# Kernel optimization log

Measured on AMD Instinct MI355X. Metric: run time of the kernel, lower is better.

The kernel has to match this reference:

```python
import jax, jax.numpy as jnp
import numpy as np

DIM = 1024
N_HEADS = 16
HEAD_DIM = DIM // N_HEADS
EPS = 1e-05
ROPE_BASE = 1000000.0


def apply_rope(x, base=ROPE_BASE):
    # x: [b, seq, heads, head_dim]
    b, seq, n_heads, dim = x.shape
    half = dim // 2
    i = jnp.arange(half)
    theta = 1.0 / base ** (2 * i / dim)
    pos = jnp.arange(seq)
    angles = pos[:, None] * theta[None, :]            # [seq, half]
    cos = jnp.cos(angles)[None, :, None, :]           # [1, seq, 1, half]
    sin = jnp.sin(angles)[None, :, None, :]
    x1, x2 = jnp.split(x, 2, axis=-1)
    return jnp.concatenate([x1 * cos - x2 * sin, x1 * sin + x2 * cos], axis=-1)


def setup_inputs() -> dict:
    key = jax.random.key(0)
    ks = jax.random.split(key, 6)
    b, seq = 2, 2048
    scale = 1.0 / np.sqrt(DIM)
    x = jax.random.normal(ks[0], (b, seq, DIM), dtype=jnp.float32)
    w_norm = jnp.ones((DIM,), dtype=jnp.float32)
    Wq = jax.random.normal(ks[1], (DIM, DIM), dtype=jnp.float32) * scale
    Wk = jax.random.normal(ks[2], (DIM, DIM), dtype=jnp.float32) * scale
    Wv = jax.random.normal(ks[3], (DIM, DIM), dtype=jnp.float32) * scale
    Wo = jax.random.normal(ks[4], (DIM, DIM), dtype=jnp.float32) * scale
    return {"x": x, "w_norm": w_norm, "Wq": Wq, "Wk": Wk, "Wv": Wv, "Wo": Wo}


def reference(x, w_norm, Wq, Wk, Wv, Wo):
    b, seq, d = x.shape
    # RMSNorm
    rms = jnp.sqrt(jnp.mean(x * x, axis=-1, keepdims=True) + EPS)
    x_norm = x / rms * w_norm
    # QKV projections (Dense without bias: y = x @ W)
    q = (x_norm @ Wq).reshape(b, seq, N_HEADS, HEAD_DIM)
    k = (x_norm @ Wk).reshape(b, seq, N_HEADS, HEAD_DIM)
    v = (x_norm @ Wv).reshape(b, seq, N_HEADS, HEAD_DIM)
    q = apply_rope(q)
    k = apply_rope(k)
    # Causal attention with full [b,h,t,s] scores (faithful to source)
    scores = jnp.einsum('bthd,bshd->bhts', q, k) / jnp.sqrt(jnp.float32(HEAD_DIM))
    causal = jnp.triu(jnp.full((seq, seq), -jnp.inf, dtype=scores.dtype), k=1)
    scores = scores + causal[None, None, :, :]
    attn = jax.nn.softmax(scores, axis=-1)
    out = jnp.einsum('bhts,bshd->bthd', attn, v).reshape(b, seq, d)
    return out @ Wo
```

## Files before the change

### kernel.cpp

```cpp
#include <hip/hip_runtime.h>

#define DIM 1024
#define SEQ 2048
#define BATCH 2
#define NHEADS 16
#define HD 64
#define ROWS (BATCH * SEQ)

typedef __bf16 bf16x8 __attribute__((ext_vector_type(8)));
typedef __bf16 bf16x4 __attribute__((ext_vector_type(4)));
typedef float f32x4 __attribute__((ext_vector_type(4)));
typedef float f32x16 __attribute__((ext_vector_type(16)));
typedef unsigned u32x4 __attribute__((ext_vector_type(4)));

__device__ __forceinline__ f32x4 f4zero() {
    f32x4 z = {0.f, 0.f, 0.f, 0.f};
    return z;
}

__device__ __forceinline__ unsigned cvtpk(float lo, float hi) {
    unsigned r;
    asm("v_cvt_pk_bf16_f32 %0, %1, %2" : "=v"(r) : "v"(lo), "v"(hi));
    return r;
}

__device__ __forceinline__ void pl32swap(unsigned& a, unsigned& b) {
    asm volatile("v_permlane32_swap_b32 %0, %1" : "+v"(a), "+v"(b));
}

#define GLOAD_LDS16(g, l)                                                                  \
    __builtin_amdgcn_global_load_lds((const __attribute__((address_space(1))) void*)(g),   \
                                     (__attribute__((address_space(3))) void*)(l), 16, 0, 0)

__global__ __launch_bounds__(256) void rmsnorm_bf16(const float* __restrict__ x,
                                                    const float* __restrict__ w,
                                                    __bf16* __restrict__ xn) {
    int row = blockIdx.x;
    int t = threadIdx.x;
    float4 v = ((const float4*)(x + (size_t)row * DIM))[t];
    float ss = v.x * v.x + v.y * v.y + v.z * v.z + v.w * v.w;
#pragma unroll
    for (int off = 1; off < 64; off <<= 1) ss += __shfl_xor(ss, off);
    __shared__ float red[4];
    if ((t & 63) == 0) red[t >> 6] = ss;
    __syncthreads();
    ss = red[0] + red[1] + red[2] + red[3];
    float scale = rsqrtf(ss * (1.0f / DIM) + 1e-5f);
    float4 wv = ((const float4*)w)[t];
    bf16x4 o;
    o[0] = (__bf16)(v.x * scale * wv.x);
    o[1] = (__bf16)(v.y * scale * wv.y);
    o[2] = (__bf16)(v.z * scale * wv.z);
    o[3] = (__bf16)(v.w * scale * wv.w);
    *(bf16x4*)(xn + (size_t)row * DIM + t * 4) = o;
}

__global__ __launch_bounds__(256) void wcvt_kernel(const float* __restrict__ Wq,
                                                   const float* __restrict__ Wk,
                                                   const float* __restrict__ Wv,
                                                   const float* __restrict__ Wo,
                                                   __bf16* tq, __bf16* tk, __bf16* tv, __bf16* to_) {
    int z = blockIdx.z;
    const float* W = z == 0 ? Wq : z == 1 ? Wk : z == 2 ? Wv : Wo;
    __bf16* T = z == 0 ? tq : z == 1 ? tk : z == 2 ? tv : to_;
    __shared__ float tile[32][33];
    int n0 = blockIdx.x * 32, k0 = blockIdx.y * 32;
    int tx = threadIdx.x & 31, ty = threadIdx.x >> 5;
#pragma unroll
    for (int j = 0; j < 32; j += 8) tile[ty + j][tx] = W[(size_t)(k0 + ty + j) * DIM + n0 + tx];
    __syncthreads();
#pragma unroll
    for (int j = 0; j < 32; j += 8)
        T[(size_t)(n0 + ty + j) * DIM + k0 + tx] = (__bf16)tile[tx][ty + j];
}

__global__ __launch_bounds__(256) void rope_table_kernel(float* __restrict__ cosT,
                                                         float* __restrict__ sinT) {
    int idx = blockIdx.x * 256 + threadIdx.x;
    int s = idx >> 5, i = idx & 31;
    float e = (2.0f * (float)i) / 64.0f;
    float theta = 1.0f / powf(1000000.0f, e);
    float ang = (float)s * theta;
    cosT[idx] = cosf(ang);
    sinT[idx] = sinf(ang);
}

__device__ __forceinline__ void gemm_core(const __bf16* __restrict__ A,
                                          const __bf16* __restrict__ Bt,
                                          int K, __bf16* As, __bf16* Bs,
                                          f32x4 (&acc)[4][4], int row0, int col0) {
    int tid = threadIdx.x;
    int w = tid >> 6, l = tid & 63, l15 = l & 15, g = l >> 4;
    int wr = (w >> 1) << 6, wc = (w & 1) << 6;

    int sr0 = tid >> 2;
    int sr1 = 64 + (tid >> 2);
    int lc0 = (((tid & 3) ^ ((tid >> 3) & 3)) << 3);
    const __bf16* gA0 = A + (size_t)(row0 + sr0) * K + lc0;
    const __bf16* gA1 = A + (size_t)(row0 + sr1) * K + lc0;
    const __bf16* gB0 = Bt + (size_t)(col0 + sr0) * K + lc0;
    const __bf16* gB1 = Bt + (size_t)(col0 + sr1) * K + lc0;
    __bf16* lA0 = As + w * 512;
    __bf16* lA1 = As + 2048 + w * 512;
    __bf16* lB0 = Bs + w * 512;
    __bf16* lB1 = Bs + 2048 + w * 512;

    int rca = ((g ^ ((l15 >> 1) & 3)) << 3);

#pragma unroll
    for (int i = 0; i < 4; ++i)
#pragma unroll
        for (int j = 0; j < 4; ++j) acc[i][j] = f4zero();

    for (int k0 = 0; k0 < K; k0 += 32) {
        __syncthreads();
        GLOAD_LDS16(gA0 + k0, lA0);
        GLOAD_LDS16(gA1 + k0, lA1);
        GLOAD_LDS16(gB0 + k0, lB0);
        GLOAD_LDS16(gB1 + k0, lB1);
        __syncthreads();

        bf16x8 af[4], bfr[4];
#pragma unroll
        for (int i = 0; i < 4; ++i) af[i] = *(const bf16x8*)&As[(wr + i * 16 + l15) * 32 + rca];
#pragma unroll
        for (int j = 0; j < 4; ++j) bfr[j] = *(const bf16x8*)&Bs[(wc + j * 16 + l15) * 32 + rca];
        __builtin_amdgcn_s_setprio(1);
#pragma unroll
        for (int i = 0; i < 4; ++i)
#pragma unroll
            for (int j = 0; j < 4; ++j)
                acc[i][j] = __builtin_amdgcn_mfma_f32_16x16x32_bf16(af[i], bfr[j], acc[i][j], 0, 0, 0);
        __builtin_amdgcn_s_setprio(0);
    }
}

__global__ __launch_bounds__(256) void gemm_qkv_kernel(const __bf16* __restrict__ xn,
                                                       const __bf16* __restrict__ wq,
                                                       const __bf16* __restrict__ wk,
                                                       const __bf16* __restrict__ wv,
                                                       __bf16* __restrict__ qo,
                                                       __bf16* __restrict__ ko,
                                                       __bf16* __restrict__ vt,
                                                       const float* __restrict__ cosT,
                                                       const float* __restrict__ sinT) {
    __shared__ __bf16 As[128 * 32];
    __shared__ __bf16 Bs[128 * 32];
    int bid = blockIdx.x;
    int tid = threadIdx.x;
    int w = tid >> 6, l = tid & 63, l15 = l & 15, g = l >> 4;
    int wr = (w >> 1) << 6, wc = (w & 1) << 6;
    f32x4 acc[4][4];

    if (bid < 512) {
        int z = bid >> 8, t = bid & 255;
        int col0 = (t & 7) << 7, row0 = (t >> 3) << 7;
        gemm_core(xn, z ? wk : wq, DIM, As, Bs, acc, row0, col0);
        __bf16* C = z ? ko : qo;
        int colbase = col0 + wc;
#pragma unroll
        for (int i = 0; i < 4; ++i) {
#pragma unroll
            for (int r = 0; r < 4; ++r) {
                int row = row0 + wr + i * 16 + g * 4 + r;
                int s = row & (SEQ - 1);
#pragma unroll
                for (int j = 0; j < 2; ++j) {
                    float c = cosT[s * 32 + j * 16 + l15];
                    float sn = sinT[s * 32 + j * 16 + l15];
                    float x1 = acc[i][j][r], x2 = acc[i][j + 2][r];
                    C[(size_t)row * DIM + colbase + j * 16 + l15] = (__bf16)(x1 * c - x2 * sn);
                    C[(size_t)row * DIM + colbase + (j + 2) * 16 + l15] = (__bf16)(x1 * sn + x2 * c);
                }
            }
        }
    } else {
        int t = bid - 512;
        int b = t >> 7, r7 = t & 127;
        int row0 = (r7 >> 4) << 7;
        int col0 = (r7 & 15) << 7;
        gemm_core(wv, xn + (size_t)b * SEQ * DIM, DIM, As, Bs, acc, row0, col0);
        __bf16* C = vt + (size_t)b * (NHEADS * HD) * SEQ;
#pragma unroll
        for (int i = 0; i < 4; ++i)
#pragma unroll
            for (int j = 0; j < 4; ++j)
#pragma unroll
                for (int r = 0; r < 4; ++r) {
                    int row = row0 + wr + i * 16 + g * 4 + r;
                    int col = col0 + wc + j * 16 + l15;
                    C[(size_t)row * SEQ + col] = (__bf16)acc[i][j][r];
                }
    }
}

__global__ __launch_bounds__(256) void gemm_out_kernel(const __bf16* __restrict__ ctx,
                                                       const __bf16* __restrict__ wo,
                                                       float* __restrict__ out) {
    __shared__ __bf16 As[128 * 32];
    __shared__ __bf16 Bs[128 * 32];
    int row0 = (int)blockIdx.y << 7, col0 = (int)blockIdx.x << 7;
    f32x4 acc[4][4];
    gemm_core(ctx, wo, DIM, As, Bs, acc, row0, col0);
    int tid = threadIdx.x;
    int w = tid >> 6, l = tid & 63, l15 = l & 15, g = l >> 4;
    int wr = (w >> 1) << 6, wc = (w & 1) << 6;
#pragma unroll
    for (int i = 0; i < 4; ++i)
#pragma unroll
        for (int j = 0; j < 4; ++j)
#pragma unroll
            for (int r = 0; r < 4; ++r) {
                int row = row0 + wr + i * 16 + g * 4 + r;
                int col = col0 + wc + j * 16 + l15;
                out[(size_t)row * DIM + col] = acc[i][j][r];
            }
}

__global__ __launch_bounds__(128) void attn_mfma_kernel(const __bf16* __restrict__ q,
                                                        const __bf16* __restrict__ k,
                                                        const __bf16* __restrict__ vt,
                                                        __bf16* __restrict__ ctx) {
    int bh = blockIdx.x;
    int qb = 31 - (int)blockIdx.y;
    int b = bh >> 4, h = bh & 15;
    __shared__ __bf16 Ks[64][72];
    __shared__ __bf16 Vs[64][72];
    int tid = threadIdx.x, w = tid >> 6, l = tid & 63;
    int l31 = l & 31, hi = l >> 5;
    size_t hoff = (size_t)(b * SEQ) * DIM + h * HD;
    const __bf16* vth = vt + (size_t)bh * HD * SEQ;
    int qw0 = qb * 64 + w * 32;
    int qrow = qw0 + l31;
    int nst = qb + 1;

    bf16x8 qf[4];
    const float c2 = 0.125f * 1.44269504f;
#pragma unroll
    for (int g = 0; g < 4; ++g) {
        bf16x8 t0 = *(const bf16x8*)&q[hoff + (size_t)qrow * DIM + g * 16 + hi * 8];
#pragma unroll
        for (int e = 0; e < 8; ++e) qf[g][e] = (__bf16)((float)t0[e] * c2);
    }

    f32x16 oA, oB;
#pragma unroll
    for (int r = 0; r < 16; ++r) {
        oA[r] = 0.f;
        oB[r] = 0.f;
    }
    float m_run = -1e30f, l_run = 0.f;

    int sr = tid >> 3, sc = (tid & 7) * 8;
    bf16x8 rk[4], rv[4];
#pragma unroll
    for (int c = 0; c < 4; ++c) {
        rk[c] = *(const bf16x8*)&k[hoff + (size_t)(c * 16 + sr) * DIM + sc];
        rv[c] = *(const bf16x8*)&vth[(size_t)(c * 16 + sr) * SEQ + sc];
    }

    for (int st = 0; st < nst; ++st) {
        int s0 = st << 6;
        __syncthreads();
#pragma unroll
        for (int c = 0; c < 4; ++c) {
            *(bf16x8*)&Ks[c * 16 + sr][sc] = rk[c];
            *(bf16x8*)&Vs[c * 16 + sr][sc] = rv[c];
        }
        __syncthreads();
        if (st + 1 < nst) {
            int sn = s0 + 64;
#pragma unroll
            for (int c = 0; c < 4; ++c) {
                rk[c] = *(const bf16x8*)&k[hoff + (size_t)(sn + c * 16 + sr) * DIM + sc];
                rv[c] = *(const bf16x8*)&vth[(size_t)(c * 16 + sr) * SEQ + sn + sc];
            }
        }

        f32x16 sa, sb;
#pragma unroll
        for (int r = 0; r < 16; ++r) {
            sa[r] = 0.f;
            sb[r] = 0.f;
        }
        __builtin_amdgcn_s_setprio(1);
#pragma unroll
        for (int g = 0; g < 4; ++g) {
            bf16x8 ka = *(const bf16x8*)&Ks[l31][g * 16 + hi * 8];
            bf16x8 kb2 = *(const bf16x8*)&Ks[32 + l31][g * 16 + hi * 8];
            sa = __builtin_amdgcn_mfma_f32_32x32x16_bf16(ka, qf[g], sa, 0, 0, 0);
            sb = __builtin_amdgcn_mfma_f32_32x32x16_bf16(kb2, qf[g], sb, 0, 0, 0);
        }
        __builtin_amdgcn_s_setprio(0);

        if (s0 + 63 > qw0) {
#pragma unroll
            for (int r = 0; r < 16; ++r) {
                int kg = s0 + (r & 3) + 8 * (r >> 2) + 4 * hi;
                if (kg > qrow) sa[r] = -1e30f;
                if (kg + 32 > qrow) sb[r] = -1e30f;
            }
        }

        float lmax = -3e38f;
#pragma unroll
        for (int r = 0; r < 16; ++r) lmax = fmaxf(lmax, fmaxf(sa[r], sb[r]));
        if (!__all(lmax <= m_run + 10.0f)) {
            float omax = fmaxf(lmax, __shfl_xor(lmax, 32));
            float m_new = fmaxf(m_run, omax);
            float alpha = exp2f(m_run - m_new);
            l_run *= alpha;
#pragma unroll
            for (int r = 0; r < 16; ++r) {
                oA[r] *= alpha;
                oB[r] *= alpha;
            }
            m_run = m_new;
        }
        float ls = 0.f;
#pragma unroll
        for (int r = 0; r < 16; ++r) {
            sa[r] = exp2f(sa[r] - m_run);
            ls += sa[r];
            sb[r] = exp2f(sb[r] - m_run);
            ls += sb[r];
        }
        l_run += ls + __shfl_xor(ls, 32);

        bf16x8 pa[4];
#pragma unroll
        for (int g = 0; g < 2; ++g) {
            unsigned a_ = cvtpk(sa[8 * g + 0], sa[8 * g + 1]);
            unsigned b_ = cvtpk(sa[8 * g + 4], sa[8 * g + 5]);
            pl32swap(a_, b_);
            unsigned c_ = cvtpk(sa[8 * g + 2], sa[8 * g + 3]);
            unsigned d_ = cvtpk(sa[8 * g + 6], sa[8 * g + 7]);
            pl32swap(c_, d_);
            u32x4 t4 = {a_, c_, b_, d_};
            pa[g] = __builtin_bit_cast(bf16x8, t4);
        }
#pragma unroll
        for (int g = 0; g < 2; ++g) {
            unsigned a_ = cvtpk(sb[8 * g + 0], sb[8 * g + 1]);
            unsigned b_ = cvtpk(sb[8 * g + 4], sb[8 * g + 5]);
            pl32swap(a_, b_);
            unsigned c_ = cvtpk(sb[8 * g + 2], sb[8 * g + 3]);
            unsigned d_ = cvtpk(sb[8 * g + 6], sb[8 * g + 7]);
            pl32swap(c_, d_);
            u32x4 t4 = {a_, c_, b_, d_};
            pa[2 + g] = __builtin_bit_cast(bf16x8, t4);
        }

        __builtin_amdgcn_s_setprio(1);
#pragma unroll
        for (int ks = 0; ks < 4; ++ks) {
            bf16x8 va = *(const bf16x8*)&Vs[l31][ks * 16 + hi * 8];
            bf16x8 vb2 = *(const bf16x8*)&Vs[32 + l31][ks * 16 + hi * 8];
            oA = __builtin_amdgcn_mfma_f32_32x32x16_bf16(va, pa[ks], oA, 0, 0, 0);
            oB = __builtin_amdgcn_mfma_f32_32x32x16_bf16(vb2, pa[ks], oB, 0, 0, 0);
        }
        __builtin_amdgcn_s_setprio(0);
    }

    float inv = 1.0f / l_run;
#pragma unroll
    for (int rr = 0; rr < 16; rr += 4) {
        int d = 8 * (rr >> 2) + 4 * hi;
        uint2 pA = {cvtpk(oA[rr] * inv, oA[rr + 1] * inv), cvtpk(oA[rr + 2] * inv, oA[rr + 3] * inv)};
        uint2 pB = {cvtpk(oB[rr] * inv, oB[rr + 1] * inv), cvtpk(oB[rr + 2] * inv, oB[rr + 3] * inv)};
        *(uint2*)&ctx[hoff + (size_t)qrow * DIM + d] = pA;
        *(uint2*)&ctx[hoff + (size_t)qrow * DIM + 32 + d] = pB;
    }
}

extern "C" void kernel_launch(void* const* d_in, const int* in_sizes, int n_in,
                              void* d_out, int out_size, void* d_ws, size_t ws_size,
                              hipStream_t stream) {
    const float* x = (const float*)d_in[0];
    const float* w_norm = (const float*)d_in[1];
    const float* Wq = (const float*)d_in[2];
    const float* Wk = (const float*)d_in[3];
    const float* Wv = (const float*)d_in[4];
    const float* Wo = (const float*)d_in[5];
    float* out = (float*)d_out;
    char* w8 = (char*)d_ws;

    __bf16* xn = (__bf16*)(w8);
    __bf16* wtq = (__bf16*)(w8 + (8ull << 20));
    __bf16* wtk = (__bf16*)(w8 + (10ull << 20));
    __bf16* wtv = (__bf16*)(w8 + (12ull << 20));
    __bf16* wto = (__bf16*)(w8 + (14ull << 20));
    __bf16* qb = (__bf16*)(w8 + (16ull << 20));
    __bf16* kb = (__bf16*)(w8 + (24ull << 20));
    __bf16* vtb = (__bf16*)(w8 + (32ull << 20));
    __bf16* ctx = (__bf16*)(w8 + (40ull << 20));
    float* cosT = (float*)(w8 + (48ull << 20));
    float* sinT = cosT + SEQ * 32;

    wcvt_kernel<<<dim3(32, 32, 4), 256, 0, stream>>>(Wq, Wk, Wv, Wo, wtq, wtk, wtv, wto);
    rmsnorm_bf16<<<ROWS, 256, 0, stream>>>(x, w_norm, xn);
    rope_table_kernel<<<(SEQ * 32) / 256, 256, 0, stream>>>(cosT, sinT);

    gemm_qkv_kernel<<<768, 256, 0, stream>>>(xn, wtq, wtk, wtv, qb, kb, vtb, cosT, sinT);

    attn_mfma_kernel<<<dim3(BATCH * NHEADS, SEQ / 64), 128, 0, stream>>>(qb, kb, vtb, ctx);

    gemm_out_kernel<<<dim3(DIM / 128, ROWS / 128), 256, 0, stream>>>(ctx, wto, out);
}
```

Baseline: 137.5 us.

## Split causal attention KV range into chunks with a separate combine kernel

Each query block's causal key range is split into chunks of up to 8 key tiles. The grid grows from 32 to 80 slots per head, so the longest block does at most 8 tiles instead of up to 32, which evens out the causal load imbalance. A new combine kernel merges the unnormalized bf16 partial outputs using their per-row max and sum statistics. The cost is an extra launch, about 20MB of partial writes and reads, a workspace layout that reuses the xn and weight-buffer regions, and some precision loss from storing unnormalized partials in bf16.

```diff
diff --git a/kernel.cpp b/kernel.cpp
--- a/kernel.cpp
+++ b/kernel.cpp
@@ -26,6 +26,13 @@
 
 __device__ __forceinline__ void pl32swap(unsigned& a, unsigned& b) {
     asm volatile("v_permlane32_swap_b32 %0, %1" : "+v"(a), "+v"(b));
+}
+
+__device__ __forceinline__ int slot_base(int qb) {
+    if (qb < 8) return qb;
+    if (qb < 16) return 8 + 2 * (qb - 8);
+    if (qb < 24) return 24 + 3 * (qb - 16);
+    return 48 + 4 * (qb - 24);
 }
 
 #define GLOAD_LDS16(g, l)                                                                  \
@@ -220,9 +227,19 @@
 __global__ __launch_bounds__(128) void attn_mfma_kernel(const __bf16* __restrict__ q,
                                                         const __bf16* __restrict__ k,
                                                         const __bf16* __restrict__ vt,
-                                                        __bf16* __restrict__ ctx) {
+                                                        __bf16* __restrict__ part_O,
+                                                        float* __restrict__ part_ml) {
     int bh = blockIdx.x;
-    int qb = 31 - (int)blockIdx.y;
+    int slot = 79 - (int)blockIdx.y;
+    int qb, ci;
+    if (slot < 8) { qb = slot; ci = 0; }
+    else if (slot < 24) { int t = slot - 8; qb = 8 + (t >> 1); ci = t & 1; }
+    else if (slot < 48) { int t = slot - 24; qb = 16 + t / 3; ci = t - 3 * (qb - 16); }
+    else { int t = slot - 48; qb = 24 + (t >> 2); ci = t & 3; }
+    int nch = (qb >> 3) + 1;
+    int ntiles = (ci == nch - 1) ? (qb + 1 - (ci << 3)) : 8;
+    int ks0 = ci << 9;
+
     int b = bh >> 4, h = bh & 15;
     __shared__ __bf16 Ks[64][72];
     __shared__ __bf16 Vs[64][72];
@@ -232,7 +249,6 @@
     const __bf16* vth = vt + (size_t)bh * HD * SEQ;
     int qw0 = qb * 64 + w * 32;
     int qrow = qw0 + l31;
-    int nst = qb + 1;
 
     bf16x8 qf[4];
     const float c2 = 0.125f * 1.44269504f;
@@ -255,12 +271,12 @@
     bf16x8 rk[4], rv[4];
 #pragma unroll
     for (int c = 0; c < 4; ++c) {
-        rk[c] = *(const bf16x8*)&k[hoff + (size_t)(c * 16 + sr) * DIM + sc];
-        rv[c] = *(const bf16x8*)&vth[(size_t)(c * 16 + sr) * SEQ + sc];
-    }
-
-    for (int st = 0; st < nst; ++st) {
-        int s0 = st << 6;
+        rk[c] = *(const bf16x8*)&k[hoff + (size_t)(ks0 + c * 16 + sr) * DIM + sc];
+        rv[c] = *(const bf16x8*)&vth[(size_t)(c * 16 + sr) * SEQ + ks0 + sc];
+    }
+
+    for (int st = 0; st < ntiles; ++st) {
+        int s0 = ks0 + (st << 6);
         __syncthreads();
 #pragma unroll
         for (int c = 0; c < 4; ++c) {
@@ -268,7 +284,7 @@
             *(bf16x8*)&Vs[c * 16 + sr][sc] = rv[c];
         }
         __syncthreads();
-        if (st + 1 < nst) {
+        if (st + 1 < ntiles) {
             int sn = s0 + 64;
 #pragma unroll
             for (int c = 0; c < 4; ++c) {
@@ -362,15 +378,72 @@
         __builtin_amdgcn_s_setprio(0);
     }
 
-    float inv = 1.0f / l_run;
+    int gslot = bh * 80 + slot;
+    int qloc = w * 32 + l31;
+    __bf16* po = part_O + (size_t)gslot * 4096 + qloc * 64;
 #pragma unroll
     for (int rr = 0; rr < 16; rr += 4) {
-        int d = 8 * (rr >> 2) + 4 * hi;
-        uint2 pA = {cvtpk(oA[rr] * inv, oA[rr + 1] * inv), cvtpk(oA[rr + 2] * inv, oA[rr + 3] * inv)};
-        uint2 pB = {cvtpk(oB[rr] * inv, oB[rr + 1] * inv), cvtpk(oB[rr + 2] * inv, oB[rr + 3] * inv)};
-        *(uint2*)&ctx[hoff + (size_t)qrow * DIM + d] = pA;
-        *(uint2*)&ctx[hoff + (size_t)qrow * DIM + 32 + d] = pB;
-    }
+        int d0 = 8 * (rr >> 2) + 4 * hi;
+        uint2 pA = {cvtpk(oA[rr], oA[rr + 1]), cvtpk(oA[rr + 2], oA[rr + 3])};
+        uint2 pB = {cvtpk(oB[rr], oB[rr + 1]), cvtpk(oB[rr + 2], oB[rr + 3])};
+        *(uint2*)&po[d0] = pA;
+        *(uint2*)&po[32 + d0] = pB;
+    }
+    if (hi == 0) {
+        part_ml[(size_t)gslot * 128 + qloc] = m_run;
+        part_ml[(size_t)gslot * 128 + 64 + qloc] = l_run;
+    }
+}
+
+__global__ __launch_bounds__(256) void attn_combine_kernel(const __bf16* __restrict__ part_O,
+                                                           const float* __restrict__ part_ml,
+                                                           __bf16* __restrict__ ctx) {
+    int bh = blockIdx.x, qb = blockIdx.y;
+    int b = bh >> 4, h = bh & 15;
+    int nch = (qb >> 3) + 1;
+    int base = slot_base(qb);
+    size_t so = (size_t)bh * 80 + base;
+    int t = threadIdx.x;
+    int row = t >> 2, dseg = (t & 3) << 4;
+
+    float mv0 = -1e30f, mv1 = -1e30f, mv2 = -1e30f, mv3 = -1e30f;
+    mv0 = part_ml[(so + 0) * 128 + row];
+    if (nch > 1) mv1 = part_ml[(so + 1) * 128 + row];
+    if (nch > 2) mv2 = part_ml[(so + 2) * 128 + row];
+    if (nch > 3) mv3 = part_ml[(so + 3) * 128 + row];
+    float mmax = fmaxf(fmaxf(mv0, mv1), fmaxf(mv2, mv3));
+
+    float acc[16];
+#pragma unroll
+    for (int e = 0; e < 16; ++e) acc[e] = 0.f;
+    float lsum = 0.f;
+
+#pragma unroll 4
+    for (int i = 0; i < 4; ++i) {
+        if (i >= nch) break;
+        float mi = i == 0 ? mv0 : i == 1 ? mv1 : i == 2 ? mv2 : mv3;
+        float wsc = exp2f(mi - mmax);
+        lsum += wsc * part_ml[(so + i) * 128 + 64 + row];
+        const __bf16* po = part_O + (so + i) * 4096 + row * 64 + dseg;
+        bf16x8 a = *(const bf16x8*)po;
+        bf16x8 b2 = *(const bf16x8*)(po + 8);
+#pragma unroll
+        for (int e = 0; e < 8; ++e) {
+            acc[e] += wsc * (float)a[e];
+            acc[8 + e] += wsc * (float)b2[e];
+        }
+    }
+
+    float inv = 1.0f / lsum;
+    bf16x8 oa, ob;
+#pragma unroll
+    for (int e = 0; e < 8; ++e) {
+        oa[e] = (__bf16)(acc[e] * inv);
+        ob[e] = (__bf16)(acc[8 + e] * inv);
+    }
+    size_t off = ((size_t)(b * SEQ) + qb * 64 + row) * DIM + h * HD + dseg;
+    *(bf16x8*)&ctx[off] = oa;
+    *(bf16x8*)&ctx[off + 8] = ob;
 }
 
 extern "C" void kernel_launch(void* const* d_in, const int* in_sizes, int n_in,
@@ -385,17 +458,20 @@
     float* out = (float*)d_out;
     char* w8 = (char*)d_ws;
 
+    const size_t MB = 1ull << 20;
     __bf16* xn = (__bf16*)(w8);
-    __bf16* wtq = (__bf16*)(w8 + (8ull << 20));
-    __bf16* wtk = (__bf16*)(w8 + (10ull << 20));
-    __bf16* wtv = (__bf16*)(w8 + (12ull << 20));
-    __bf16* wto = (__bf16*)(w8 + (14ull << 20));
-    __bf16* qb = (__bf16*)(w8 + (16ull << 20));
-    __bf16* kb = (__bf16*)(w8 + (24ull << 20));
-    __bf16* vtb = (__bf16*)(w8 + (32ull << 20));
-    __bf16* ctx = (__bf16*)(w8 + (40ull << 20));
-    float* cosT = (float*)(w8 + (48ull << 20));
+    __bf16* wtq = (__bf16*)(w8 + 8 * MB);
+    __bf16* wtk = (__bf16*)(w8 + 10 * MB);
+    __bf16* wtv = (__bf16*)(w8 + 12 * MB);
+    __bf16* part_O = (__bf16*)(w8);
+    __bf16* wto = (__bf16*)(w8 + 20 * MB);
+    __bf16* qb = (__bf16*)(w8 + 22 * MB);
+    __bf16* kb = (__bf16*)(w8 + 30 * MB);
+    __bf16* vtb = (__bf16*)(w8 + 38 * MB);
+    __bf16* ctx = (__bf16*)(w8 + 46 * MB);
+    float* cosT = (float*)(w8 + 54 * MB);
     float* sinT = cosT + SEQ * 32;
+    float* part_ml = (float*)(w8 + 55 * MB);
 
     wcvt_kernel<<<dim3(32, 32, 4), 256, 0, stream>>>(Wq, Wk, Wv, Wo, wtq, wtk, wtv, wto);
     rmsnorm_bf16<<<ROWS, 256, 0, stream>>>(x, w_norm, xn);
@@ -403,7 +479,8 @@
 
     gemm_qkv_kernel<<<768, 256, 0, stream>>>(xn, wtq, wtk, wtv, qb, kb, vtb, cosT, sinT);
 
-    attn_mfma_kernel<<<dim3(BATCH * NHEADS, SEQ / 64), 128, 0, stream>>>(qb, kb, vtb, ctx);
+    attn_mfma_kernel<<<dim3(BATCH * NHEADS, 80), 128, 0, stream>>>(qb, kb, vtb, part_O, part_ml);
+    attn_combine_kernel<<<dim3(BATCH * NHEADS, SEQ / 64), 256, 0, stream>>>(part_O, part_ml, ctx);
 
     gemm_out_kernel<<<dim3(DIM / 128, ROWS / 128), 256, 0, stream>>>(ctx, wto, out);
 }
```

Measured after the change: 134.2 us. 2.4% less time.

## Enlarge attention blocks to 256 query rows with double-buffered shared K/V tiles

Applied to the files above, without the earlier changes.

The attention kernel now runs 8 waves (512 threads) per block covering 256 query rows, so one set of K/V tiles staged in shared memory is reused by four times as many queries. K/V staging is double-buffered, with a prefetch two tiles ahead, which leaves one barrier per tile. Waves whose causal range ends earlier skip the compute but still take part in loads and barriers. The grid drops from 1024 to 256 blocks, and the reversed heavy-first ordering is removed. This can cause load imbalance, because a block's cost grows with its query index.

```diff
diff --git a/kernel.cpp b/kernel.cpp
--- a/kernel.cpp
+++ b/kernel.cpp
@@ -217,30 +217,34 @@
             }
 }
 
-__global__ __launch_bounds__(128) void attn_mfma_kernel(const __bf16* __restrict__ q,
-                                                        const __bf16* __restrict__ k,
-                                                        const __bf16* __restrict__ vt,
-                                                        __bf16* __restrict__ ctx) {
+__global__ __launch_bounds__(512) void attn_fused_kernel(const __bf16* __restrict__ q,
+                                                         const __bf16* __restrict__ k,
+                                                         const __bf16* __restrict__ vt,
+                                                         __bf16* __restrict__ ctx) {
     int bh = blockIdx.x;
-    int qb = 31 - (int)blockIdx.y;
+    int qb = blockIdx.y;
     int b = bh >> 4, h = bh & 15;
-    __shared__ __bf16 Ks[64][72];
-    __shared__ __bf16 Vs[64][72];
+    __shared__ __bf16 Ks[2][64][72];
+    __shared__ __bf16 Vs[2][64][72];
     int tid = threadIdx.x, w = tid >> 6, l = tid & 63;
     int l31 = l & 31, hi = l >> 5;
     size_t hoff = (size_t)(b * SEQ) * DIM + h * HD;
     const __bf16* vth = vt + (size_t)bh * HD * SEQ;
-    int qw0 = qb * 64 + w * 32;
+    int qw0 = qb * 256 + w * 32;
     int qrow = qw0 + l31;
-    int nst = qb + 1;
+    int ntiles = 4 * qb + 4;
+    int mytiles = 4 * qb + (w >> 1) + 1;
 
     bf16x8 qf[4];
-    const float c2 = 0.125f * 1.44269504f;
-#pragma unroll
-    for (int g = 0; g < 4; ++g) {
-        bf16x8 t0 = *(const bf16x8*)&q[hoff + (size_t)qrow * DIM + g * 16 + hi * 8];
-#pragma unroll
-        for (int e = 0; e < 8; ++e) qf[g][e] = (__bf16)((float)t0[e] * c2);
+    {
+        const __bf16* qptr = q + hoff + (size_t)qrow * DIM + hi * 8;
+        const float c2 = 0.125f * 1.44269504f;
+#pragma unroll
+        for (int g = 0; g < 4; ++g) {
+            bf16x8 t0 = *(const bf16x8*)(qptr + g * 16);
+#pragma unroll
+            for (int e = 0; e < 8; ++e) qf[g][e] = (__bf16)((float)t0[e] * c2);
+        }
     }
 
     f32x16 oA, oB;
@@ -251,115 +255,120 @@
     }
     float m_run = -1e30f, l_run = 0.f;
 
-    int sr = tid >> 3, sc = (tid & 7) * 8;
-    bf16x8 rk[4], rv[4];
-#pragma unroll
-    for (int c = 0; c < 4; ++c) {
-        rk[c] = *(const bf16x8*)&k[hoff + (size_t)(c * 16 + sr) * DIM + sc];
-        rv[c] = *(const bf16x8*)&vth[(size_t)(c * 16 + sr) * SEQ + sc];
-    }
-
-    for (int st = 0; st < nst; ++st) {
-        int s0 = st << 6;
-        __syncthreads();
-#pragma unroll
-        for (int c = 0; c < 4; ++c) {
-            *(bf16x8*)&Ks[c * 16 + sr][sc] = rk[c];
-            *(bf16x8*)&Vs[c * 16 + sr][sc] = rv[c];
+    int srow = tid >> 3, scol = (tid & 7) * 8;
+    const __bf16* kst = k + hoff + (size_t)srow * DIM + scol;
+    const __bf16* vst = vth + (size_t)srow * SEQ + scol;
+
+    bf16x8 kr = *(const bf16x8*)kst;
+    bf16x8 vr = *(const bf16x8*)vst;
+    *(bf16x8*)&Ks[0][srow][scol] = kr;
+    *(bf16x8*)&Vs[0][srow][scol] = vr;
+    kr = *(const bf16x8*)(kst + (size_t)64 * DIM);
+    vr = *(const bf16x8*)(vst + 64);
+    __syncthreads();
+
+    for (int st = 0; st < ntiles; ++st) {
+        int cur = st & 1;
+        bf16x8 kn, vn;
+        if (st + 2 < ntiles) {
+            kn = *(const bf16x8*)(kst + (size_t)((st + 2) * 64) * DIM);
+            vn = *(const bf16x8*)(vst + (st + 2) * 64);
+        }
+
+        if (st < mytiles) {
+            int s0 = st << 6;
+            f32x16 sa, sb;
+#pragma unroll
+            for (int r = 0; r < 16; ++r) {
+                sa[r] = 0.f;
+                sb[r] = 0.f;
+            }
+            __builtin_amdgcn_s_setprio(1);
+#pragma unroll
+            for (int g = 0; g < 4; ++g) {
+                bf16x8 ka = *(const bf16x8*)&Ks[cur][l31][g * 16 + hi * 8];
+                bf16x8 kb2 = *(const bf16x8*)&Ks[cur][32 + l31][g * 16 + hi * 8];
+                sa = __builtin_amdgcn_mfma_f32_32x32x16_bf16(ka, qf[g], sa, 0, 0, 0);
+                sb = __builtin_amdgcn_mfma_f32_32x32x16_bf16(kb2, qf[g], sb, 0, 0, 0);
+            }
+            __builtin_amdgcn_s_setprio(0);
+
+            if (s0 + 63 > qw0) {
+#pragma unroll
+                for (int r = 0; r < 16; ++r) {
+                    int kg = s0 + (r & 3) + 8 * (r >> 2) + 4 * hi;
+                    if (kg > qrow) sa[r] = -1e30f;
+                    if (kg + 32 > qrow) sb[r] = -1e30f;
+                }
+            }
+
+            float lmax = -3e38f;
+#pragma unroll
+            for (int r = 0; r < 16; ++r) lmax = fmaxf(lmax, fmaxf(sa[r], sb[r]));
+            if (!__all(lmax <= m_run + 10.0f)) {
+                float omax = fmaxf(lmax, __shfl_xor(lmax, 32));
+                float m_new = fmaxf(m_run, omax);
+                float alpha = exp2f(m_run - m_new);
+                l_run *= alpha;
+#pragma unroll
+                for (int r = 0; r < 16; ++r) {
+                    oA[r] *= alpha;
+                    oB[r] *= alpha;
+                }
+                m_run = m_new;
+            }
+            float ls = 0.f;
+#pragma unroll
+            for (int r = 0; r < 16; ++r) {
+                sa[r] = exp2f(sa[r] - m_run);
+                ls += sa[r];
+                sb[r] = exp2f(sb[r] - m_run);
+                ls += sb[r];
+            }
+            l_run += ls + __shfl_xor(ls, 32);
+
+            bf16x8 pa[4];
+#pragma unroll
+            for (int g = 0; g < 2; ++g) {
+                unsigned a_ = cvtpk(sa[8 * g + 0], sa[8 * g + 1]);
+                unsigned b_ = cvtpk(sa[8 * g + 4], sa[8 * g + 5]);
+                pl32swap(a_, b_);
+                unsigned c_ = cvtpk(sa[8 * g + 2], sa[8 * g + 3]);
+                unsigned d_ = cvtpk(sa[8 * g + 6], sa[8 * g + 7]);
+                pl32swap(c_, d_);
+                u32x4 t4 = {a_, c_, b_, d_};
+                pa[g] = __builtin_bit_cast(bf16x8, t4);
+            }
+#pragma unroll
+            for (int g = 0; g < 2; ++g) {
+                unsigned a_ = cvtpk(sb[8 * g + 0], sb[8 * g + 1]);
+                unsigned b_ = cvtpk(sb[8 * g + 4], sb[8 * g + 5]);
+                pl32swap(a_, b_);
+                unsigned c_ = cvtpk(sb[8 * g + 2], sb[8 * g + 3]);
+                unsigned d_ = cvtpk(sb[8 * g + 6], sb[8 * g + 7]);
+                pl32swap(c_, d_);
+                u32x4 t4 = {a_, c_, b_, d_};
+                pa[2 + g] = __builtin_bit_cast(bf16x8, t4);
+            }
+
+            __builtin_amdgcn_s_setprio(1);
+#pragma unroll
+            for (int ks = 0; ks < 4; ++ks) {
+                bf16x8 va = *(const bf16x8*)&Vs[cur][l31][ks * 16 + hi * 8];
+                bf16x8 vb2 = *(const bf16x8*)&Vs[cur][32 + l31][ks * 16 + hi * 8];
+                oA = __builtin_amdgcn_mfma_f32_32x32x16_bf16(va, pa[ks], oA, 0, 0, 0);
+                oB = __builtin_amdgcn_mfma_f32_32x32x16_bf16(vb2, pa[ks], oB, 0, 0, 0);
+            }
+            __builtin_amdgcn_s_setprio(0);
+        }
+
+        if (st + 1 < ntiles) {
+            *(bf16x8*)&Ks[cur ^ 1][srow][scol] = kr;
+            *(bf16x8*)&Vs[cur ^ 1][srow][scol] = vr;
+            kr = kn;
+            vr = vn;
         }
         __syncthreads();
-        if (st + 1 < nst) {
-            int sn = s0 + 64;
-#pragma unroll
-            for (int c = 0; c < 4; ++c) {
-                rk[c] = *(const bf16x8*)&k[hoff + (size_t)(sn + c * 16 + sr) * DIM + sc];
-                rv[c] = *(const bf16x8*)&vth[(size_t)(c * 16 + sr) * SEQ + sn + sc];
-            }
-        }
-
-        f32x16 sa, sb;
-#pragma unroll
-        for (int r = 0; r < 16; ++r) {
-            sa[r] = 0.f;
-            sb[r] = 0.f;
-        }
-        __builtin_amdgcn_s_setprio(1);
-#pragma unroll
-        for (int g = 0; g < 4; ++g) {
-            bf16x8 ka = *(const bf16x8*)&Ks[l31][g * 16 + hi * 8];
-            bf16x8 kb2 = *(const bf16x8*)&Ks[32 + l31][g * 16 + hi * 8];
-            sa = __builtin_amdgcn_mfma_f32_32x32x16_bf16(ka, qf[g], sa, 0, 0, 0);
-            sb = __builtin_amdgcn_mfma_f32_32x32x16_bf16(kb2, qf[g], sb, 0, 0, 0);
-        }
-        __builtin_amdgcn_s_setprio(0);
-
-        if (s0 + 63 > qw0) {
-#pragma unroll
-            for (int r = 0; r < 16; ++r) {
-                int kg = s0 + (r & 3) + 8 * (r >> 2) + 4 * hi;
-                if (kg > qrow) sa[r] = -1e30f;
-                if (kg + 32 > qrow) sb[r] = -1e30f;
-            }
-        }
-
-        float lmax = -3e38f;
-#pragma unroll
-        for (int r = 0; r < 16; ++r) lmax = fmaxf(lmax, fmaxf(sa[r], sb[r]));
-        if (!__all(lmax <= m_run + 10.0f)) {
-            float omax = fmaxf(lmax, __shfl_xor(lmax, 32));
-            float m_new = fmaxf(m_run, omax);
-            float alpha = exp2f(m_run - m_new);
-            l_run *= alpha;
-#pragma unroll
-            for (int r = 0; r < 16; ++r) {
-                oA[r] *= alpha;
-                oB[r] *= alpha;
-            }
-            m_run = m_new;
-        }
-        float ls = 0.f;
-#pragma unroll
-        for (int r = 0; r < 16; ++r) {
-            sa[r] = exp2f(sa[r] - m_run);
-            ls += sa[r];
-            sb[r] = exp2f(sb[r] - m_run);
-            ls += sb[r];
-        }
-        l_run += ls + __shfl_xor(ls, 32);
-
-        bf16x8 pa[4];
-#pragma unroll
-        for (int g = 0; g < 2; ++g) {
-            unsigned a_ = cvtpk(sa[8 * g + 0], sa[8 * g + 1]);
-            unsigned b_ = cvtpk(sa[8 * g + 4], sa[8 * g + 5]);
-            pl32swap(a_, b_);
-            unsigned c_ = cvtpk(sa[8 * g + 2], sa[8 * g + 3]);
-            unsigned d_ = cvtpk(sa[8 * g + 6], sa[8 * g + 7]);
-            pl32swap(c_, d_);
-            u32x4 t4 = {a_, c_, b_, d_};
-            pa[g] = __builtin_bit_cast(bf16x8, t4);
-        }
-#pragma unroll
-        for (int g = 0; g < 2; ++g) {
-            unsigned a_ = cvtpk(sb[8 * g + 0], sb[8 * g + 1]);
-            unsigned b_ = cvtpk(sb[8 * g + 4], sb[8 * g + 5]);
-            pl32swap(a_, b_);
-            unsigned c_ = cvtpk(sb[8 * g + 2], sb[8 * g + 3]);
-            unsigned d_ = cvtpk(sb[8 * g + 6], sb[8 * g + 7]);
-            pl32swap(c_, d_);
-            u32x4 t4 = {a_, c_, b_, d_};
-            pa[2 + g] = __builtin_bit_cast(bf16x8, t4);
-        }
-
-        __builtin_amdgcn_s_setprio(1);
-#pragma unroll
-        for (int ks = 0; ks < 4; ++ks) {
-            bf16x8 va = *(const bf16x8*)&Vs[l31][ks * 16 + hi * 8];
-            bf16x8 vb2 = *(const bf16x8*)&Vs[32 + l31][ks * 16 + hi * 8];
-            oA = __builtin_amdgcn_mfma_f32_32x32x16_bf16(va, pa[ks], oA, 0, 0, 0);
-            oB = __builtin_amdgcn_mfma_f32_32x32x16_bf16(vb2, pa[ks], oB, 0, 0, 0);
-        }
-        __builtin_amdgcn_s_setprio(0);
     }
 
     float inv = 1.0f / l_run;
@@ -385,16 +394,17 @@
     float* out = (float*)d_out;
     char* w8 = (char*)d_ws;
 
+    const size_t MB = 1ull << 20;
     __bf16* xn = (__bf16*)(w8);
-    __bf16* wtq = (__bf16*)(w8 + (8ull << 20));
-    __bf16* wtk = (__bf16*)(w8 + (10ull << 20));
-    __bf16* wtv = (__bf16*)(w8 + (12ull << 20));
-    __bf16* wto = (__bf16*)(w8 + (14ull << 20));
-    __bf16* qb = (__bf16*)(w8 + (16ull << 20));
-    __bf16* kb = (__bf16*)(w8 + (24ull << 20));
-    __bf16* vtb = (__bf16*)(w8 + (32ull << 20));
-    __bf16* ctx = (__bf16*)(w8 + (40ull << 20));
-    float* cosT = (float*)(w8 + (48ull << 20));
+    __bf16* wtq = (__bf16*)(w8 + 8 * MB);
+    __bf16* wtk = (__bf16*)(w8 + 10 * MB);
+    __bf16* wtv = (__bf16*)(w8 + 12 * MB);
+    __bf16* wto = (__bf16*)(w8 + 14 * MB);
+    __bf16* qb = (__bf16*)(w8 + 16 * MB);
+    __bf16* kb = (__bf16*)(w8 + 24 * MB);
+    __bf16* vtb = (__bf16*)(w8 + 32 * MB);
+    __bf16* ctx = (__bf16*)(w8 + 40 * MB);
+    float* cosT = (float*)(w8 + 48 * MB);
     float* sinT = cosT + SEQ * 32;
 
     wcvt_kernel<<<dim3(32, 32, 4), 256, 0, stream>>>(Wq, Wk, Wv, Wo, wtq, wtk, wtv, wto);
@@ -403,7 +413,7 @@
 
     gemm_qkv_kernel<<<768, 256, 0, stream>>>(xn, wtq, wtk, wtv, qb, kb, vtb, cosT, sinT);
 
-    attn_mfma_kernel<<<dim3(BATCH * NHEADS, SEQ / 64), 128, 0, stream>>>(qb, kb, vtb, ctx);
+    attn_fused_kernel<<<dim3(BATCH * NHEADS, SEQ / 256), 512, 0, stream>>>(qb, kb, vtb, ctx);
 
     gemm_out_kernel<<<dim3(DIM / 128, ROWS / 128), 256, 0, stream>>>(ctx, wto, out);
 }
```

New measurement: 144.4 us. 1.05x slower.
